# Optimization experiments

Measured on AMD Instinct MI355X. Metric: run time of the kernel, lower is better.

Reference implementation:

```python
import jax, jax.numpy as jnp
import numpy as np

N, E, DIN, H, OUT = 100000, 1600000, 64, 128, 2
BN_EPS = 1e-5


def _mlp_bn(h, wa, ba, g, be, wb, bb):
    # PyG MLP([d_in, H, H]): lin -> batch_norm (train-mode batch stats) -> relu -> lin (plain last)
    h = h @ wa + ba
    mu = jnp.mean(h, axis=0)
    var = jnp.mean((h - mu) ** 2, axis=0)  # biased var, as in BatchNorm training
    h = g * (h - mu) * jax.lax.rsqrt(var + BN_EPS) + be
    h = jax.nn.relu(h)
    return h @ wb + bb


def _gin_layer(x, src, dst, wa, ba, g, be, wb, bb, eps):
    # sum-aggregate neighbor features: agg[i] = sum_{(j->i) in E} x[j]
    agg = jax.ops.segment_sum(x[src], dst, num_segments=N)
    h = (1.0 + eps) * x + agg
    h = _mlp_bn(h, wa, ba, g, be, wb, bb)
    return jax.nn.relu(h)  # GIN.forward outer activation (dropout p=0)


def setup_inputs() -> dict:
    key = jax.random.key(0)
    ks = iter(jax.random.split(key, 40))
    d = {}
    d['x'] = jax.random.normal(next(ks), (N, DIN), dtype=jnp.float32)
    d['edge_index'] = jax.random.randint(next(ks), (2, E), 0, N, dtype=jnp.int64)

    def lin(k, fi, fo):
        return jax.random.normal(k, (fi, fo), dtype=jnp.float32) * (1.0 / np.sqrt(fi))

    fin = DIN
    for l in range(3):
        d[f'w{l}a'] = lin(next(ks), fin, H)
        d[f'b{l}a'] = jnp.zeros((H,), jnp.float32)
        d[f'g{l}'] = jnp.ones((H,), jnp.float32)
        d[f'be{l}'] = jnp.zeros((H,), jnp.float32)
        d[f'w{l}b'] = lin(next(ks), H, H)
        d[f'b{l}b'] = jnp.zeros((H,), jnp.float32)
        d[f'eps{l}'] = jnp.zeros((), jnp.float32)
        fin = H
    d['hwa'] = lin(next(ks), H, H)
    d['hba'] = jnp.zeros((H,), jnp.float32)
    d['hwb'] = lin(next(ks), H, OUT)
    d['hbb'] = jnp.zeros((OUT,), jnp.float32)
    return d


def reference(x, edge_index,
              w0a, b0a, g0, be0, w0b, b0b, eps0,
              w1a, b1a, g1, be1, w1b, b1b, eps1,
              w2a, b2a, g2, be2, w2b, b2b, eps2,
              hwa, hba, hwb, hbb):
    src, dst = edge_index[0], edge_index[1]
    h = _gin_layer(x, src, dst, w0a, b0a, g0, be0, w0b, b0b, eps0)
    h = _gin_layer(h, src, dst, w1a, b1a, g1, be1, w1b, b1b, eps1)
    h = _gin_layer(h, src, dst, w2a, b2a, g2, be2, w2b, b2b, eps2)
    # head MLP([H, H, OUT], norm=None, dropout=0): lin -> relu -> lin
    h = jax.nn.relu(h @ hwa + hba)
    return h @ hwb + hbb
```

## Files before the change

kernel.cpp:

```cpp
#include <hip/hip_runtime.h>

#define NN 100000
#define NE 1600000
#define HD 128
#define GG  782
#define NBKT 391
#define BW_SH 8

typedef unsigned short u16;
typedef __attribute__((ext_vector_type(8))) short bf16x8;
typedef __attribute__((ext_vector_type(4))) float f32x4;

__device__ __forceinline__ u16 f2b(float f) {
    unsigned u = __builtin_bit_cast(unsigned, f);
    unsigned r = (u + 0x7FFFu + ((u >> 16) & 1u)) >> 16;
    return (u16)r;
}
__device__ __forceinline__ float b2f(u16 h) {
    unsigned u = ((unsigned)h) << 16;
    return __builtin_bit_cast(float, u);
}
__device__ __forceinline__ float lof(unsigned v) {
    return __builtin_bit_cast(float, v << 16);
}
__device__ __forceinline__ float hif(unsigned v) {
    return __builtin_bit_cast(float, v & 0xFFFF0000u);
}
__device__ __forceinline__ unsigned pack2(float a, float b) {
    return (unsigned)f2b(a) | ((unsigned)f2b(b) << 16);
}

__global__ __launch_bounds__(256)
void k_bcount(const int* __restrict__ dst, int* __restrict__ bucketCnt) {
    __shared__ int cnt[NBKT];
    const int t = threadIdx.x;
    for (int i = t; i < NBKT; i += 256) cnt[i] = 0;
    __syncthreads();
    int e0 = blockIdx.x * 4096 + t;
    #pragma unroll
    for (int i = 0; i < 16; ++i) {
        int e = e0 + i * 256;
        if (e < NE) atomicAdd(&cnt[dst[e] >> BW_SH], 1);
    }
    __syncthreads();
    for (int i = t; i < NBKT; i += 256)
        if (cnt[i]) atomicAdd(bucketCnt + i, cnt[i]);
}

__global__ __launch_bounds__(512)
void k_bscan(const int* __restrict__ bucketCnt, int* __restrict__ bucketBase,
             int* __restrict__ bucketCur) {
    __shared__ int s[512];
    const int t = threadIdx.x;
    int v = (t < NBKT) ? bucketCnt[t] : 0;
    s[t] = v;
    __syncthreads();
    #pragma unroll
    for (int off = 1; off < 512; off <<= 1) {
        int tmp = (t >= off) ? s[t - off] : 0;
        __syncthreads();
        s[t] += tmp;
        __syncthreads();
    }
    if (t < NBKT) {
        bucketBase[t + 1] = s[t];
        bucketCur[t] = s[t] - v;
        if (t == 0) bucketBase[0] = 0;
    }
}

__global__ __launch_bounds__(256)
void k_bscatter(const int* __restrict__ src, const int* __restrict__ dst,
                int* __restrict__ bucketCur, int2* __restrict__ pairs) {
    __shared__ int cnt[NBKT];
    __shared__ int cbase[NBKT];
    const int t = threadIdx.x;
    for (int i = t; i < NBKT; i += 256) cnt[i] = 0;
    __syncthreads();
    int e0 = blockIdx.x * 4096 + t;
    int db[16];
    #pragma unroll
    for (int i = 0; i < 16; ++i) {
        int e = e0 + i * 256;
        db[i] = (e < NE) ? dst[e] : -1;
        if (db[i] >= 0) atomicAdd(&cnt[db[i] >> BW_SH], 1);
    }
    __syncthreads();
    for (int i = t; i < NBKT; i += 256)
        cbase[i] = cnt[i] ? atomicAdd(bucketCur + i, cnt[i]) : 0;
    __syncthreads();
    for (int i = t; i < NBKT; i += 256) cnt[i] = 0;
    __syncthreads();
    #pragma unroll
    for (int i = 0; i < 16; ++i) {
        int e = e0 + i * 256;
        if (e < NE) {
            int b = db[i] >> BW_SH;
            int r = atomicAdd(&cnt[b], 1);
            pairs[cbase[b] + r] = make_int2(src[e], db[i]);
        }
    }
}

__global__ __launch_bounds__(256)
void k_bfinal(const int2* __restrict__ pairs, const int* __restrict__ bucketBase,
              int* __restrict__ rowptr, int* __restrict__ eidx) {
    __shared__ int deg[256], pfx[256], cur[256];
    const int b = blockIdx.x, t = threadIdx.x;
    const int n0 = b << BW_SH;
    const int bb = bucketBase[b], be = bucketBase[b + 1];
    deg[t] = 0;
    __syncthreads();
    for (int e = bb + t; e < be; e += 256)
        atomicAdd(&deg[pairs[e].y & 255], 1);
    __syncthreads();
    int v = deg[t];
    pfx[t] = v;
    __syncthreads();
    #pragma unroll
    for (int off = 1; off < 256; off <<= 1) {
        int tmp = (t >= off) ? pfx[t - off] : 0;
        __syncthreads();
        pfx[t] += tmp;
        __syncthreads();
    }
    int n = n0 + t;
    if (n < NN) rowptr[n + 1] = bb + pfx[t];
    if (b == 0 && t == 0) rowptr[0] = 0;
    cur[t] = bb + pfx[t] - v;
    __syncthreads();
    for (int e = bb + t; e < be; e += 256) {
        int2 p = pairs[e];
        int pos = atomicAdd(&cur[p.y & 255], 1);
        eidx[pos] = p.x;
    }
}

__global__ __launch_bounds__(256)
void k_cvt(const float* __restrict__ in, u16* __restrict__ out, int n4) {
    for (int i = blockIdx.x * 256 + threadIdx.x; i < n4; i += gridDim.x * 256) {
        float4 v = reinterpret_cast<const float4*>(in)[i];
        uint2 o;
        o.x = pack2(v.x, v.y);
        o.y = pack2(v.z, v.w);
        *reinterpret_cast<uint2*>(out + (size_t)i * 4) = o;
    }
}

template<int F>
__global__ __launch_bounds__(64)
void k_aggr(const u16* __restrict__ x, const int* __restrict__ rowptr,
            const int* __restrict__ eidx, const float* __restrict__ epsp,
            u16* __restrict__ out) {
    const int n = blockIdx.x;
    const int t = threadIdx.x;
    const int p0 = rowptr[n], p1 = rowptr[n + 1];
    const float e1 = 1.0f + epsp[0];

    if constexpr (F == 128) {
        const unsigned off = 2u * t;
        float a0 = 0.f, a1 = 0.f, c0 = 0.f, c1 = 0.f;
        int p = p0;
        for (; p + 3 < p1; p += 4) {
            unsigned v0 = *reinterpret_cast<const unsigned*>(x + (size_t)eidx[p]     * 128 + off);
            unsigned v1 = *reinterpret_cast<const unsigned*>(x + (size_t)eidx[p + 1] * 128 + off);
            unsigned v2 = *reinterpret_cast<const unsigned*>(x + (size_t)eidx[p + 2] * 128 + off);
            unsigned v3 = *reinterpret_cast<const unsigned*>(x + (size_t)eidx[p + 3] * 128 + off);
            a0 += lof(v0); a1 += hif(v0);
            c0 += lof(v1); c1 += hif(v1);
            a0 += lof(v2); a1 += hif(v2);
            c0 += lof(v3); c1 += hif(v3);
        }
        for (; p < p1; ++p) {
            unsigned v0 = *reinterpret_cast<const unsigned*>(x + (size_t)eidx[p] * 128 + off);
            a0 += lof(v0); a1 += hif(v0);
        }
        unsigned xs = *reinterpret_cast<const unsigned*>(x + (size_t)n * 128 + off);
        float o0 = fmaf(e1, lof(xs), a0 + c0);
        float o1 = fmaf(e1, hif(xs), a1 + c1);
        *reinterpret_cast<unsigned*>(out + (size_t)n * 128 + off) = pack2(o0, o1);
    } else {
        float a0 = 0.f, a1 = 0.f;
        int p = p0;
        for (; p + 3 < p1; p += 4) {
            float x0 = b2f(x[(size_t)eidx[p]     * 64 + t]);
            float x1 = b2f(x[(size_t)eidx[p + 1] * 64 + t]);
            float x2 = b2f(x[(size_t)eidx[p + 2] * 64 + t]);
            float x3 = b2f(x[(size_t)eidx[p + 3] * 64 + t]);
            a0 += x0 + x2; a1 += x1 + x3;
        }
        for (; p < p1; ++p) a0 += b2f(x[(size_t)eidx[p] * 64 + t]);
        float xs = b2f(x[(size_t)n * 64 + t]);
        out[(size_t)n * 64 + t] = f2b(fmaf(e1, xs, a0 + a1));
    }
}

template<int K, int PRO, int EPI, int OM, int ABV, int STATS>
__global__ __launch_bounds__(256)
void k_gemm(const void* __restrict__ Av,
            const float* __restrict__ af,
            const float* __restrict__ bff,
            const float* __restrict__ W,
            const float* __restrict__ bias,
            void* __restrict__ Cout,
            float* __restrict__ partial,
            const float* __restrict__ w2,
            const float* __restrict__ b2) {
    __shared__ u16 Whi[128 * K];
    __shared__ u16 Wlo[128 * K];
    __shared__ float redS[4][128];
    __shared__ float redQ[4][128];

    const int t = threadIdx.x;
    const int l = t & 63;
    const int w = t >> 6;
    const int mbase = blockIdx.x * 128 + w * 32;
    const int l15 = l & 15;
    const int lg = l >> 4;

    for (int idx = t; idx < K * 32; idx += 256) {
        int k  = idx >> 5;
        int n0 = (idx & 31) * 4;
        float4 wv = *reinterpret_cast<const float4*>(W + (size_t)k * 128 + n0);
        float wa[4] = {wv.x, wv.y, wv.z, wv.w};
        #pragma unroll
        for (int j = 0; j < 4; ++j) {
            int n = n0 + j;
            int byte = n * (2 * K) + k * 2;
            byte ^= ((n & 7) << 4);
            u16 hi = f2b(wa[j]);
            u16 lo = f2b(wa[j] - b2f(hi));
            *reinterpret_cast<u16*>(reinterpret_cast<char*>(Whi) + byte) = hi;
            *reinterpret_cast<u16*>(reinterpret_cast<char*>(Wlo) + byte) = lo;
        }
    }
    __syncthreads();

    f32x4 acc[2][8];
    #pragma unroll
    for (int i = 0; i < 2; ++i)
        #pragma unroll
        for (int j = 0; j < 8; ++j) acc[i][j] = (f32x4){0.f, 0.f, 0.f, 0.f};

    #pragma unroll
    for (int kc = 0; kc < K / 32; ++kc) {
        bf16x8 whi[8], wlo[8];
        #pragma unroll
        for (int nb = 0; nb < 8; ++nb) {
            int n = nb * 16 + l15;
            int byte = n * (2 * K) + kc * 64 + lg * 16;
            byte ^= ((n & 7) << 4);
            whi[nb] = *reinterpret_cast<const bf16x8*>(
                reinterpret_cast<const char*>(Whi) + byte);
            wlo[nb] = *reinterpret_cast<const bf16x8*>(
                reinterpret_cast<const char*>(Wlo) + byte);
        }
        float aa[8], bb[8];
        if (PRO == 1) {
            int kk = kc * 32 + lg * 8;
            float4 x0 = *reinterpret_cast<const float4*>(af + kk);
            float4 x1 = *reinterpret_cast<const float4*>(af + kk + 4);
            float4 y0 = *reinterpret_cast<const float4*>(bff + kk);
            float4 y1 = *reinterpret_cast<const float4*>(bff + kk + 4);
            aa[0] = x0.x; aa[1] = x0.y; aa[2] = x0.z; aa[3] = x0.w;
            aa[4] = x1.x; aa[5] = x1.y; aa[6] = x1.z; aa[7] = x1.w;
            bb[0] = y0.x; bb[1] = y0.y; bb[2] = y0.z; bb[3] = y0.w;
            bb[4] = y1.x; bb[5] = y1.y; bb[6] = y1.z; bb[7] = y1.w;
        }
        #pragma unroll
        for (int mb = 0; mb < 2; ++mb) {
            int m = mbase + mb * 16 + l15;
            if (ABV == 1) {
                bf16x8 ff = {};
                if (m < NN)
                    ff = *reinterpret_cast<const bf16x8*>(
                        (const u16*)Av + (size_t)m * K + kc * 32 + lg * 8);
                #pragma unroll
                for (int nb = 0; nb < 8; ++nb) {
                    acc[mb][nb] = __builtin_amdgcn_mfma_f32_16x16x32_bf16(
                        whi[nb], ff, acc[mb][nb], 0, 0, 0);
                    acc[mb][nb] = __builtin_amdgcn_mfma_f32_16x16x32_bf16(
                        wlo[nb], ff, acc[mb][nb], 0, 0, 0);
                }
            } else {
                float av[8] = {0.f, 0.f, 0.f, 0.f, 0.f, 0.f, 0.f, 0.f};
                if (m < NN) {
                    const float* ap = (const float*)Av + (size_t)m * K + kc * 32 + lg * 8;
                    float4 x0 = *reinterpret_cast<const float4*>(ap);
                    float4 x1 = *reinterpret_cast<const float4*>(ap + 4);
                    av[0] = x0.x; av[1] = x0.y; av[2] = x0.z; av[3] = x0.w;
                    av[4] = x1.x; av[5] = x1.y; av[6] = x1.z; av[7] = x1.w;
                }
                if (PRO == 1) {
                    #pragma unroll
                    for (int j = 0; j < 8; ++j)
                        av[j] = fmaxf(fmaf(aa[j], av[j], bb[j]), 0.f);
                }
                union { bf16x8 v; u16 s[8]; } uh, ul;
                #pragma unroll
                for (int j = 0; j < 8; ++j) {
                    u16 hi = f2b(av[j]);
                    uh.s[j] = hi;
                    ul.s[j] = f2b(av[j] - b2f(hi));
                }
                #pragma unroll
                for (int nb = 0; nb < 8; ++nb) {
                    acc[mb][nb] = __builtin_amdgcn_mfma_f32_16x16x32_bf16(
                        whi[nb], uh.v, acc[mb][nb], 0, 0, 0);
                    acc[mb][nb] = __builtin_amdgcn_mfma_f32_16x16x32_bf16(
                        whi[nb], ul.v, acc[mb][nb], 0, 0, 0);
                    acc[mb][nb] = __builtin_amdgcn_mfma_f32_16x16x32_bf16(
                        wlo[nb], uh.v, acc[mb][nb], 0, 0, 0);
                }
            }
        }
    }

    if (OM == 2) {
        float o00 = 0.f, o01 = 0.f, o10 = 0.f, o11 = 0.f;
        #pragma unroll
        for (int nb = 0; nb < 8; ++nb) {
            int n0 = nb * 16 + lg * 4;
            float4 b4 = *reinterpret_cast<const float4*>(bias + n0);
            float bv[4] = {b4.x, b4.y, b4.z, b4.w};
            #pragma unroll
            for (int r = 0; r < 4; ++r) {
                int n = n0 + r;
                float w20 = w2[n * 2], w21 = w2[n * 2 + 1];
                float v0 = fmaxf(acc[0][nb][r] + bv[r], 0.f);
                float v1 = fmaxf(acc[1][nb][r] + bv[r], 0.f);
                o00 = fmaf(v0, w20, o00); o01 = fmaf(v0, w21, o01);
                o10 = fmaf(v1, w20, o10); o11 = fmaf(v1, w21, o11);
            }
        }
        o00 += __shfl_xor(o00, 16); o00 += __shfl_xor(o00, 32);
        o01 += __shfl_xor(o01, 16); o01 += __shfl_xor(o01, 32);
        o10 += __shfl_xor(o10, 16); o10 += __shfl_xor(o10, 32);
        o11 += __shfl_xor(o11, 16); o11 += __shfl_xor(o11, 32);
        if (lg == 0) {
            float bb0 = b2[0], bb1 = b2[1];
            float* outp = (float*)Cout;
            int m0 = mbase + l15, m1 = mbase + 16 + l15;
            if (m0 < NN)
                *reinterpret_cast<float2*>(outp + (size_t)m0 * 2) =
                    make_float2(o00 + bb0, o01 + bb1);
            if (m1 < NN)
                *reinterpret_cast<float2*>(outp + (size_t)m1 * 2) =
                    make_float2(o10 + bb0, o11 + bb1);
        }
        return;
    }

    #pragma unroll
    for (int nb = 0; nb < 8; ++nb) {
        int n0 = nb * 16 + lg * 4;
        float4 b4 = *reinterpret_cast<const float4*>(bias + n0);
        float bv[4] = {b4.x, b4.y, b4.z, b4.w};
        float vs[2][4];
        #pragma unroll
        for (int mb = 0; mb < 2; ++mb) {
            int m = mbase + mb * 16 + l15;
            #pragma unroll
            for (int r = 0; r < 4; ++r)
                vs[mb][r] = (m < NN) ? (acc[mb][nb][r] + bv[r]) : 0.f;
        }
        if (STATS == 1) {
            #pragma unroll
            for (int r = 0; r < 4; ++r) {
                float s = vs[0][r] + vs[1][r];
                float q = vs[0][r] * vs[0][r] + vs[1][r] * vs[1][r];
                s += __shfl_xor(s, 1); q += __shfl_xor(q, 1);
                s += __shfl_xor(s, 2); q += __shfl_xor(q, 2);
                s += __shfl_xor(s, 4); q += __shfl_xor(q, 4);
                s += __shfl_xor(s, 8); q += __shfl_xor(q, 8);
                if (l15 == 0) {
                    int n = n0 + r;
                    redS[w][n] = s;
                    redQ[w][n] = q;
                }
            }
        }
        #pragma unroll
        for (int mb = 0; mb < 2; ++mb) {
            int m = mbase + mb * 16 + l15;
            if (m >= NN) continue;
            float v0 = vs[mb][0], v1 = vs[mb][1], v2 = vs[mb][2], v3 = vs[mb][3];
            if (EPI == 1) {
                v0 = fmaxf(v0, 0.f); v1 = fmaxf(v1, 0.f);
                v2 = fmaxf(v2, 0.f); v3 = fmaxf(v3, 0.f);
            }
            if (OM == 1) {
                uint2 o;
                o.x = pack2(v0, v1);
                o.y = pack2(v2, v3);
                *reinterpret_cast<uint2*>((u16*)Cout + (size_t)m * 128 + n0) = o;
            } else {
                float4 o = make_float4(v0, v1, v2, v3);
                *reinterpret_cast<float4*>((float*)Cout + (size_t)m * 128 + n0) = o;
            }
        }
    }

    if (STATS == 1) {
        __syncthreads();
        if (t < 128) {
            float s = redS[0][t] + redS[1][t] + redS[2][t] + redS[3][t];
            float q = redQ[0][t] + redQ[1][t] + redQ[2][t] + redQ[3][t];
            partial[(size_t)blockIdx.x * 256 + t] = s;
            partial[(size_t)blockIdx.x * 256 + 128 + t] = q;
        }
    }
}

__global__ __launch_bounds__(256)
void k_bnfin2(const float* __restrict__ partial,
              const float* __restrict__ g, const float* __restrict__ be,
              float* __restrict__ af, float* __restrict__ bf) {
    const int c = blockIdx.x;
    const int t = threadIdx.x;
    __shared__ double sS[256];
    __shared__ double sQ[256];
    double S = 0.0, Q = 0.0;
    for (int b = t; b < GG; b += 256) {
        S += (double)partial[(size_t)b * 256 + c];
        Q += (double)partial[(size_t)b * 256 + 128 + c];
    }
    sS[t] = S; sQ[t] = Q;
    __syncthreads();
    #pragma unroll
    for (int off = 128; off > 0; off >>= 1) {
        if (t < off) { sS[t] += sS[t + off]; sQ[t] += sQ[t + off]; }
        __syncthreads();
    }
    if (t == 0) {
        double mu  = sS[0] / (double)NN;
        double var = sQ[0] / (double)NN - mu * mu;
        double a   = (double)g[c] / sqrt(var + 1e-5);
        af[c] = (float)a;
        bf[c] = be[c] - (float)(mu * a);
    }
}

extern "C" void kernel_launch(void* const* d_in, const int* in_sizes, int n_in,
                              void* d_out, int out_size, void* d_ws, size_t ws_size,
                              hipStream_t stream) {
    const float* x  = (const float*)d_in[0];
    const int*   ei = (const int*)d_in[1];
    const int* src = ei;
    const int* dst = ei + NE;
    auto P = [&](int i) { return (const float*)d_in[i]; };

    const size_t BUFF = (size_t)NN * HD * sizeof(float);
    const size_t BUFH = (size_t)NN * HD * sizeof(u16);
    char* ws = (char*)d_ws;
    u16*   gB   = (u16*)(ws);
    u16*   aggB = (u16*)(ws + BUFH);
    float* yF   = (float*)(ws + 2 * BUFH);
    float* hF   = (float*)(ws + 2 * BUFH + BUFF);
    u16*   xb   = (u16*)(ws + 2 * BUFH + 2 * BUFF);
    char*  sb   = ws + 2 * BUFH + 2 * BUFF + (size_t)NN * 64 * sizeof(u16);
    float* partial = (float*)sb;
    float* af = (float*)(sb + (size_t)GG * 256 * 4);
    float* bf = af + 128;
    int* bucketCnt  = (int*)(af + 256);
    int* bucketBase = bucketCnt + NBKT + 1;
    int* bucketCur  = bucketBase + NBKT + 1;
    int* rowptr     = bucketCur + NBKT + 1;
    int* eidx       = rowptr + NN + 3;
    int2* pairs     = (int2*)(((size_t)(eidx + NE) + 15) & ~(size_t)15);

    const int EBLK = (NE + 4095) / 4096;

    hipMemsetAsync(bucketCnt, 0, NBKT * sizeof(int), stream);
    k_bcount<<<EBLK, 256, 0, stream>>>(dst, bucketCnt);
    k_bscan<<<1, 512, 0, stream>>>(bucketCnt, bucketBase, bucketCur);
    k_bscatter<<<EBLK, 256, 0, stream>>>(src, dst, bucketCur, pairs);
    k_bfinal<<<NBKT, 256, 0, stream>>>(pairs, bucketBase, rowptr, eidx);

    k_cvt<<<2048, 256, 0, stream>>>(x, xb, NN * 64 / 4);

    k_aggr<64><<<NN, 64, 0, stream>>>(xb, rowptr, eidx, P(8), aggB);
    k_gemm<64, 0, 0, 0, 1, 1><<<GG, 256, 0, stream>>>(
        aggB, nullptr, nullptr, P(2), P(3), yF, partial, nullptr, nullptr);
    k_bnfin2<<<128, 256, 0, stream>>>(partial, P(4), P(5), af, bf);
    k_gemm<128, 1, 1, 1, 0, 0><<<GG, 256, 0, stream>>>(
        yF, af, bf, P(6), P(7), gB, nullptr, nullptr, nullptr);

    k_aggr<128><<<NN, 64, 0, stream>>>(gB, rowptr, eidx, P(15), aggB);
    k_gemm<128, 0, 0, 0, 1, 1><<<GG, 256, 0, stream>>>(
        aggB, nullptr, nullptr, P(9), P(10), yF, partial, nullptr, nullptr);
    k_bnfin2<<<128, 256, 0, stream>>>(partial, P(11), P(12), af, bf);
    k_gemm<128, 1, 1, 1, 0, 0><<<GG, 256, 0, stream>>>(
        yF, af, bf, P(13), P(14), gB, nullptr, nullptr, nullptr);

    k_aggr<128><<<NN, 64, 0, stream>>>(gB, rowptr, eidx, P(22), aggB);
    k_gemm<128, 0, 0, 0, 1, 1><<<GG, 256, 0, stream>>>(
        aggB, nullptr, nullptr, P(16), P(17), yF, partial, nullptr, nullptr);
    k_bnfin2<<<128, 256, 0, stream>>>(partial, P(18), P(19), af, bf);
    k_gemm<128, 1, 1, 0, 0, 0><<<GG, 256, 0, stream>>>(
        yF, af, bf, P(20), P(21), hF, nullptr, nullptr, nullptr);

    k_gemm<128, 0, 1, 2, 0, 0><<<GG, 256, 0, stream>>>(
        hF, nullptr, nullptr, P(23), P(24), (float*)d_out, nullptr, P(25), P(26));
}
```

Before: 711.9 us.

## Pre-split weights into fragment layout once; pack 4 nodes per aggregation block

```diff
diff --git a/kernel.cpp b/kernel.cpp
--- a/kernel.cpp
+++ b/kernel.cpp
@@ -147,51 +147,105 @@
     }
 }
 
+__global__ __launch_bounds__(256)
+void k_wprep(const float* __restrict__ wa, const float* __restrict__ wb,
+             const float* __restrict__ wc, const float* __restrict__ wd,
+             const float* __restrict__ we, const float* __restrict__ wf,
+             const float* __restrict__ wg, u16* __restrict__ out) {
+    const float* Ws[7] = {wa, wb, wc, wd, we, wf, wg};
+    const int    Ks[7] = {64, 128, 128, 128, 128, 128, 128};
+    const int m = blockIdx.y;
+    const int id = blockIdx.x * 256 + threadIdx.x;
+    const int K = Ks[m];
+    if (id >= K * 128) return;
+    int j  = id & 7;
+    int nb = (id >> 3) & 7;
+    int l  = (id >> 6) & 63;
+    int kc = id >> 12;
+    int n = nb * 16 + (l & 15);
+    int k = kc * 32 + ((l >> 4) & 3) * 8 + j;
+    float w = Ws[m][(size_t)k * 128 + n];
+    u16 hi = f2b(w);
+    u16 lo = f2b(w - b2f(hi));
+    out[(size_t)m * 32768 + id] = hi;
+    out[(size_t)m * 32768 + 16384 + id] = lo;
+}
+
 template<int F>
-__global__ __launch_bounds__(64)
+__global__ __launch_bounds__(256)
 void k_aggr(const u16* __restrict__ x, const int* __restrict__ rowptr,
             const int* __restrict__ eidx, const float* __restrict__ epsp,
             u16* __restrict__ out) {
-    const int n = blockIdx.x;
-    const int t = threadIdx.x;
+    const int t  = threadIdx.x;
+    const int wv = t >> 6;
+    const int l  = t & 63;
+    const int h  = l >> 5;
+    const int c  = l & 31;
+    const int n  = blockIdx.x * 4 + wv;
+    if (n >= NN) return;
     const int p0 = rowptr[n], p1 = rowptr[n + 1];
     const float e1 = 1.0f + epsp[0];
+    const int hcnt = (p1 - p0 + 1) >> 1;
+    const int ph0 = p0 + (h ? hcnt : 0);
+    const int ph1 = h ? p1 : (p0 + hcnt);
 
     if constexpr (F == 128) {
-        const unsigned off = 2u * t;
-        float a0 = 0.f, a1 = 0.f, c0 = 0.f, c1 = 0.f;
-        int p = p0;
-        for (; p + 3 < p1; p += 4) {
-            unsigned v0 = *reinterpret_cast<const unsigned*>(x + (size_t)eidx[p]     * 128 + off);
-            unsigned v1 = *reinterpret_cast<const unsigned*>(x + (size_t)eidx[p + 1] * 128 + off);
-            unsigned v2 = *reinterpret_cast<const unsigned*>(x + (size_t)eidx[p + 2] * 128 + off);
-            unsigned v3 = *reinterpret_cast<const unsigned*>(x + (size_t)eidx[p + 3] * 128 + off);
-            a0 += lof(v0); a1 += hif(v0);
-            c0 += lof(v1); c1 += hif(v1);
-            a0 += lof(v2); a1 += hif(v2);
-            c0 += lof(v3); c1 += hif(v3);
-        }
-        for (; p < p1; ++p) {
-            unsigned v0 = *reinterpret_cast<const unsigned*>(x + (size_t)eidx[p] * 128 + off);
-            a0 += lof(v0); a1 += hif(v0);
-        }
-        unsigned xs = *reinterpret_cast<const unsigned*>(x + (size_t)n * 128 + off);
-        float o0 = fmaf(e1, lof(xs), a0 + c0);
-        float o1 = fmaf(e1, hif(xs), a1 + c1);
-        *reinterpret_cast<unsigned*>(out + (size_t)n * 128 + off) = pack2(o0, o1);
+        const unsigned off = 4u * c;
+        float a0[4] = {0.f, 0.f, 0.f, 0.f}, a1[4] = {0.f, 0.f, 0.f, 0.f};
+        int p = ph0;
+        for (; p + 3 < ph1; p += 4) {
+            uint2 v0 = *reinterpret_cast<const uint2*>(x + (size_t)eidx[p]     * 128 + off);
+            uint2 v1 = *reinterpret_cast<const uint2*>(x + (size_t)eidx[p + 1] * 128 + off);
+            uint2 v2 = *reinterpret_cast<const uint2*>(x + (size_t)eidx[p + 2] * 128 + off);
+            uint2 v3 = *reinterpret_cast<const uint2*>(x + (size_t)eidx[p + 3] * 128 + off);
+            a0[0] += lof(v0.x); a0[1] += hif(v0.x); a0[2] += lof(v0.y); a0[3] += hif(v0.y);
+            a1[0] += lof(v1.x); a1[1] += hif(v1.x); a1[2] += lof(v1.y); a1[3] += hif(v1.y);
+            a0[0] += lof(v2.x); a0[1] += hif(v2.x); a0[2] += lof(v2.y); a0[3] += hif(v2.y);
+            a1[0] += lof(v3.x); a1[1] += hif(v3.x); a1[2] += lof(v3.y); a1[3] += hif(v3.y);
+        }
+        for (; p < ph1; ++p) {
+            uint2 v0 = *reinterpret_cast<const uint2*>(x + (size_t)eidx[p] * 128 + off);
+            a0[0] += lof(v0.x); a0[1] += hif(v0.x); a0[2] += lof(v0.y); a0[3] += hif(v0.y);
+        }
+        float s[4];
+        #pragma unroll
+        for (int j = 0; j < 4; ++j) {
+            s[j] = a0[j] + a1[j];
+            s[j] += __shfl_xor(s[j], 32);
+        }
+        if (h == 0) {
+            uint2 xs = *reinterpret_cast<const uint2*>(x + (size_t)n * 128 + off);
+            uint2 o;
+            o.x = pack2(fmaf(e1, lof(xs.x), s[0]), fmaf(e1, hif(xs.x), s[1]));
+            o.y = pack2(fmaf(e1, lof(xs.y), s[2]), fmaf(e1, hif(xs.y), s[3]));
+            *reinterpret_cast<uint2*>(out + (size_t)n * 128 + off) = o;
+        }
     } else {
-        float a0 = 0.f, a1 = 0.f;
-        int p = p0;
-        for (; p + 3 < p1; p += 4) {
-            float x0 = b2f(x[(size_t)eidx[p]     * 64 + t]);
-            float x1 = b2f(x[(size_t)eidx[p + 1] * 64 + t]);
-            float x2 = b2f(x[(size_t)eidx[p + 2] * 64 + t]);
-            float x3 = b2f(x[(size_t)eidx[p + 3] * 64 + t]);
-            a0 += x0 + x2; a1 += x1 + x3;
-        }
-        for (; p < p1; ++p) a0 += b2f(x[(size_t)eidx[p] * 64 + t]);
-        float xs = b2f(x[(size_t)n * 64 + t]);
-        out[(size_t)n * 64 + t] = f2b(fmaf(e1, xs, a0 + a1));
+        const unsigned off = 2u * c;
+        float a0[2] = {0.f, 0.f}, a1[2] = {0.f, 0.f};
+        int p = ph0;
+        for (; p + 3 < ph1; p += 4) {
+            unsigned v0 = *reinterpret_cast<const unsigned*>(x + (size_t)eidx[p]     * 64 + off);
+            unsigned v1 = *reinterpret_cast<const unsigned*>(x + (size_t)eidx[p + 1] * 64 + off);
+            unsigned v2 = *reinterpret_cast<const unsigned*>(x + (size_t)eidx[p + 2] * 64 + off);
+            unsigned v3 = *reinterpret_cast<const unsigned*>(x + (size_t)eidx[p + 3] * 64 + off);
+            a0[0] += lof(v0); a0[1] += hif(v0);
+            a1[0] += lof(v1); a1[1] += hif(v1);
+            a0[0] += lof(v2); a0[1] += hif(v2);
+            a1[0] += lof(v3); a1[1] += hif(v3);
+        }
+        for (; p < ph1; ++p) {
+            unsigned v0 = *reinterpret_cast<const unsigned*>(x + (size_t)eidx[p] * 64 + off);
+            a0[0] += lof(v0); a0[1] += hif(v0);
+        }
+        float s0 = a0[0] + a1[0], s1 = a0[1] + a1[1];
+        s0 += __shfl_xor(s0, 32);
+        s1 += __shfl_xor(s1, 32);
+        if (h == 0) {
+            unsigned xs = *reinterpret_cast<const unsigned*>(x + (size_t)n * 64 + off);
+            *reinterpret_cast<unsigned*>(out + (size_t)n * 64 + off) =
+                pack2(fmaf(e1, lof(xs), s0), fmaf(e1, hif(xs), s1));
+        }
     }
 }
 
@@ -200,14 +254,13 @@
 void k_gemm(const void* __restrict__ Av,
             const float* __restrict__ af,
             const float* __restrict__ bff,
-            const float* __restrict__ W,
+            const u16* __restrict__ whiG,
+            const u16* __restrict__ wloG,
             const float* __restrict__ bias,
             void* __restrict__ Cout,
             float* __restrict__ partial,
             const float* __restrict__ w2,
             const float* __restrict__ b2) {
-    __shared__ u16 Whi[128 * K];
-    __shared__ u16 Wlo[128 * K];
     __shared__ float redS[4][128];
     __shared__ float redQ[4][128];
 
@@ -218,24 +271,6 @@
     const int l15 = l & 15;
     const int lg = l >> 4;
 
-    for (int idx = t; idx < K * 32; idx += 256) {
-        int k  = idx >> 5;
-        int n0 = (idx & 31) * 4;
-        float4 wv = *reinterpret_cast<const float4*>(W + (size_t)k * 128 + n0);
-        float wa[4] = {wv.x, wv.y, wv.z, wv.w};
-        #pragma unroll
-        for (int j = 0; j < 4; ++j) {
-            int n = n0 + j;
-            int byte = n * (2 * K) + k * 2;
-            byte ^= ((n & 7) << 4);
-            u16 hi = f2b(wa[j]);
-            u16 lo = f2b(wa[j] - b2f(hi));
-            *reinterpret_cast<u16*>(reinterpret_cast<char*>(Whi) + byte) = hi;
-            *reinterpret_cast<u16*>(reinterpret_cast<char*>(Wlo) + byte) = lo;
-        }
-    }
-    __syncthreads();
-
     f32x4 acc[2][8];
     #pragma unroll
     for (int i = 0; i < 2; ++i)
@@ -244,16 +279,13 @@
 
     #pragma unroll
     for (int kc = 0; kc < K / 32; ++kc) {
+        const u16* wb = whiG + ((kc * 64 + l) << 6);
+        const u16* wl = wloG + ((kc * 64 + l) << 6);
         bf16x8 whi[8], wlo[8];
         #pragma unroll
         for (int nb = 0; nb < 8; ++nb) {
-            int n = nb * 16 + l15;
-            int byte = n * (2 * K) + kc * 64 + lg * 16;
-            byte ^= ((n & 7) << 4);
-            whi[nb] = *reinterpret_cast<const bf16x8*>(
-                reinterpret_cast<const char*>(Whi) + byte);
-            wlo[nb] = *reinterpret_cast<const bf16x8*>(
-                reinterpret_cast<const char*>(Wlo) + byte);
+            whi[nb] = *reinterpret_cast<const bf16x8*>(wb + nb * 8);
+            wlo[nb] = *reinterpret_cast<const bf16x8*>(wl + nb * 8);
         }
         float aa[8], bb[8];
         if (PRO == 1) {
@@ -462,14 +494,19 @@
     float* partial = (float*)sb;
     float* af = (float*)(sb + (size_t)GG * 256 * 4);
     float* bf = af + 128;
-    int* bucketCnt  = (int*)(af + 256);
+    u16* wsplit = (u16*)(af + 256);
+    int* bucketCnt  = (int*)(wsplit + 7 * 32768);
     int* bucketBase = bucketCnt + NBKT + 1;
     int* bucketCur  = bucketBase + NBKT + 1;
     int* rowptr     = bucketCur + NBKT + 1;
     int* eidx       = rowptr + NN + 3;
     int2* pairs     = (int2*)(((size_t)(eidx + NE) + 15) & ~(size_t)15);
 
+    auto WH = [&](int slot) { return wsplit + (size_t)slot * 32768; };
+    auto WL = [&](int slot) { return wsplit + (size_t)slot * 32768 + 16384; };
+
     const int EBLK = (NE + 4095) / 4096;
+    const int AGRID = (NN + 3) / 4;
 
     hipMemsetAsync(bucketCnt, 0, NBKT * sizeof(int), stream);
     k_bcount<<<EBLK, 256, 0, stream>>>(dst, bucketCnt);
@@ -477,29 +514,32 @@
     k_bscatter<<<EBLK, 256, 0, stream>>>(src, dst, bucketCur, pairs);
     k_bfinal<<<NBKT, 256, 0, stream>>>(pairs, bucketBase, rowptr, eidx);
 
+    k_wprep<<<dim3(64, 7), 256, 0, stream>>>(
+        P(2), P(6), P(9), P(13), P(16), P(20), P(23), wsplit);
+
     k_cvt<<<2048, 256, 0, stream>>>(x, xb, NN * 64 / 4);
 
-    k_aggr<64><<<NN, 64, 0, stream>>>(xb, rowptr, eidx, P(8), aggB);
+    k_aggr<64><<<AGRID, 256, 0, stream>>>(xb, rowptr, eidx, P(8), aggB);
     k_gemm<64, 0, 0, 0, 1, 1><<<GG, 256, 0, stream>>>(
-        aggB, nullptr, nullptr, P(2), P(3), yF, partial, nullptr, nullptr);
+        aggB, nullptr, nullptr, WH(0), WL(0), P(3), yF, partial, nullptr, nullptr);
     k_bnfin2<<<128, 256, 0, stream>>>(partial, P(4), P(5), af, bf);
     k_gemm<128, 1, 1, 1, 0, 0><<<GG, 256, 0, stream>>>(
-        yF, af, bf, P(6), P(7), gB, nullptr, nullptr, nullptr);
-
-    k_aggr<128><<<NN, 64, 0, stream>>>(gB, rowptr, eidx, P(15), aggB);
+        yF, af, bf, WH(1), WL(1), P(7), gB, nullptr, nullptr, nullptr);
+
+    k_aggr<128><<<AGRID, 256, 0, stream>>>(gB, rowptr, eidx, P(15), aggB);
     k_gemm<128, 0, 0, 0, 1, 1><<<GG, 256, 0, stream>>>(
-        aggB, nullptr, nullptr, P(9), P(10), yF, partial, nullptr, nullptr);
+        aggB, nullptr, nullptr, WH(2), WL(2), P(10), yF, partial, nullptr, nullptr);
     k_bnfin2<<<128, 256, 0, stream>>>(partial, P(11), P(12), af, bf);
     k_gemm<128, 1, 1, 1, 0, 0><<<GG, 256, 0, stream>>>(
-        yF, af, bf, P(13), P(14), gB, nullptr, nullptr, nullptr);
-
-    k_aggr<128><<<NN, 64, 0, stream>>>(gB, rowptr, eidx, P(22), aggB);
+        yF, af, bf, WH(3), WL(3), P(14), gB, nullptr, nullptr, nullptr);
+
+    k_aggr<128><<<AGRID, 256, 0, stream>>>(gB, rowptr, eidx, P(22), aggB);
     k_gemm<128, 0, 0, 0, 1, 1><<<GG, 256, 0, stream>>>(
-        aggB, nullptr, nullptr, P(16), P(17), yF, partial, nullptr, nullptr);
+        aggB, nullptr, nullptr, WH(4), WL(4), P(17), yF, partial, nullptr, nullptr);
     k_bnfin2<<<128, 256, 0, stream>>>(partial, P(18), P(19), af, bf);
     k_gemm<128, 1, 1, 0, 0, 0><<<GG, 256, 0, stream>>>(
-        yF, af, bf, P(20), P(21), hF, nullptr, nullptr, nullptr);
+        yF, af, bf, WH(5), WL(5), P(21), hF, nullptr, nullptr, nullptr);
 
     k_gemm<128, 0, 1, 2, 0, 0><<<GG, 256, 0, stream>>>(
-        hF, nullptr, nullptr, P(23), P(24), (float*)d_out, nullptr, P(25), P(26));
-}
+        hF, nullptr, nullptr, WH(6), WL(6), P(24), (float*)d_out, nullptr, P(25), P(26));
+}
```

Measured after the change: 721.3 us. Within noise of the previous version (+1.3%).
